# Performance work log

Hardware: AMD Instinct MI355X
Metric: run time of the kernel (lower is better)

The kernel has to match this reference:

```python
import jax, jax.numpy as jnp
import numpy as np

LAYERS, BLOCKS = 10, 4
RES_CH, END_CH, CLASSES, GROUPS = 32, 256, 256, 1
BN_EPS = 1e-5


def conv1x1(x, w, b):
    # x: (bn, Cin, L), w: (Cout, Cin), b: (Cout,)
    return jnp.einsum('oc,bcl->bol', w, x) + b[None, :, None]


def mish(x):
    return x * jnp.tanh(jax.nn.softplus(x))


def concat_mish(x):
    return mish(jnp.concatenate((x, -x), axis=1))


def channel_shuffle(x, groups):
    if groups == 1:
        return x
    bn, c, l = x.shape
    return x.reshape(bn, groups, c // groups, l).transpose(0, 2, 1, 3).reshape(bn, c, l)


def batchnorm_train(x, g, b):
    # BatchNorm1d in training mode: per-channel stats over (batch, length), biased var
    m = jnp.mean(x, axis=(0, 2), keepdims=True)
    v = jnp.mean((x - m) ** 2, axis=(0, 2), keepdims=True)
    return (x - m) * jax.lax.rsqrt(v + BN_EPS) * g[None, :, None] + b[None, :, None]


def dilate(x, dilation, init_dilation, pad_start=True):
    bn, c, l = x.shape
    if dilation == 1:
        x = jnp.transpose(x, (1, 2, 0)).reshape(c, l * init_dilation, bn // init_dilation)
        return jnp.transpose(x, (2, 0, 1))
    f = dilation // init_dilation
    if f == 1:
        return x
    new_l = (l + f - 1) // f * f
    if new_l != l:
        pad = (new_l - l, 0) if pad_start else (0, new_l - l)
        x = jnp.pad(x, ((0, 0), (0, 0), pad))
        l = new_l
    l //= f
    bn *= f
    x = jnp.transpose(x, (1, 2, 0)).reshape(c, l, bn)
    return jnp.transpose(x, (2, 0, 1))


def setup_inputs() -> dict:
    key = jax.random.key(0)
    ks = iter(jax.random.split(key, 32))
    nl = LAYERS * BLOCKS
    f32 = jnp.float32
    inp = {
        'x': jax.random.normal(next(ks), (8, CLASSES, 8192), dtype=f32),
        'start_w': jax.random.normal(next(ks), (RES_CH, CLASSES), dtype=f32) * 0.05,
        'start_b': jnp.zeros((RES_CH,), f32),
        'gate_w': jax.random.normal(next(ks), (nl, RES_CH // 2, RES_CH), dtype=f32) * 0.15,
        'gate_b': jnp.zeros((nl, RES_CH // 2), f32),
        'res_w': jax.random.normal(next(ks), (nl, RES_CH, RES_CH), dtype=f32) * 0.15,
        'res_b': jnp.zeros((nl, RES_CH), f32),
        'bn_g': jnp.ones((nl, RES_CH), f32),
        'bn_b': jnp.zeros((nl, RES_CH), f32),
        'end_bn1_g': jnp.ones((RES_CH,), f32),
        'end_bn1_b': jnp.zeros((RES_CH,), f32),
        'end_conv1_w': jax.random.normal(next(ks), (END_CH // 2, 2 * RES_CH), dtype=f32) * 0.1,
        'end_conv1_b': jnp.zeros((END_CH // 2,), f32),
        'end_bn2_g': jnp.ones((END_CH // 2,), f32),
        'end_bn2_b': jnp.zeros((END_CH // 2,), f32),
        'end_conv2_w': jax.random.normal(next(ks), (CLASSES, END_CH), dtype=f32) * 0.05,
        'end_conv2_b': jnp.zeros((CLASSES,), f32),
    }
    return inp


def reference(x, start_w, start_b, gate_w, gate_b, res_w, res_b, bn_g, bn_b,
              end_bn1_g, end_bn1_b, end_conv1_w, end_conv1_b,
              end_bn2_g, end_bn2_b, end_conv2_w, end_conv2_b):
    x = conv1x1(x, start_w, start_b)
    prev_dilation = 1
    i = 0
    for block in range(BLOCKS):
        for layer in range(LAYERS):
            x = dilate(x, 2 ** layer, prev_dilation)
            prev_dilation = 2 ** layer
            x0 = x
            h = concat_mish(conv1x1(x, gate_w[i], gate_b[i]))
            h = channel_shuffle(h, GROUPS)
            h = batchnorm_train(conv1x1(h, res_w[i], res_b[i]), bn_g[i], bn_b[i])
            h = channel_shuffle(h, GROUPS)
            x = x0 + h
            i += 1
    x = concat_mish(batchnorm_train(x, end_bn1_g, end_bn1_b))
    x = concat_mish(batchnorm_train(conv1x1(x, end_conv1_w, end_conv1_b), end_bn2_g, end_bn2_b))
    x = conv1x1(x, end_conv2_w, end_conv2_b)
    x = dilate(x, 1, 2 ** (LAYERS - 1))
    return x
```

## Files before the change

kernel.cpp:

```cpp
#include <hip/hip_runtime.h>

#define BS 256
#define NBLK 256
#define STATS_F   0
#define W2T_F     46080
#define XBUF_F    131072
#define RBUF_F    2228224
#define WS_NEED_BYTES (4325376ull * 4ull)
#define CNTS_U  4096

__device__ __forceinline__ void mish2(float v, float& mp, float& mn) {
  float vc = fminf(fmaxf(v, -30.f), 30.f);
  float u  = __expf(vc);
  float n1 = u * (u + 2.f);
  mp = v * n1 * __builtin_amdgcn_rcpf(n1 + 2.f);
  float n2 = fmaf(2.f, u, 1.f);
  float d2 = fmaf(2.f * u, u, n2);
  mn = -v * n2 * __builtin_amdgcn_rcpf(d2);
}

__device__ __forceinline__ float coherent_ld(const float* p) {
  return __hip_atomic_load(p, __ATOMIC_RELAXED, __HIP_MEMORY_SCOPE_AGENT);
}
__device__ __forceinline__ void coherent_st(float* p, float v) {
  __hip_atomic_store(p, v, __ATOMIC_RELAXED, __HIP_MEMORY_SCOPE_AGENT);
}

__device__ __forceinline__ void block_reduce_stats(const float (&vals)[32],
    float* s_red, float* s_p2, float* slot, int t) {
  #pragma unroll
  for (int cc = 0; cc < 8; ++cc) {
    float4 v = make_float4(vals[cc*4+0], vals[cc*4+1], vals[cc*4+2], vals[cc*4+3]);
    *(float4*)(&s_red[t*32 + ((cc ^ (t & 7)) << 2)]) = v;
  }
  __syncthreads();
  {
    int q = t & 63, grp = t >> 6, c = q & 31;
    bool issq = (q >= 32);
    float acc = 0.f;
    #pragma clang loop unroll_count(8)
    for (int rr = 0; rr < 64; ++rr) {
      int row = grp * 64 + rr;
      float v = s_red[row*32 + ((((c >> 2) ^ (row & 7)) << 2) | (c & 3))];
      acc = fmaf(v, issq ? v : 1.f, acc);
    }
    s_p2[t] = acc;
  }
  __syncthreads();
  if (t < 64) {
    float tot = s_p2[t] + s_p2[t+64] + s_p2[t+128] + s_p2[t+192];
    unsafeAtomicAdd(&slot[(blockIdx.x & 15) * 64 + t], tot);
  }
  __syncthreads();
}

__device__ __forceinline__ void bn32_from_slot(const float* slot, const float* g,
    const float* b, float* sA, float* sB, float* s_tmp, int t) {
  if (t < 64) {
    float s = 0.f;
    #pragma unroll
    for (int rep = 0; rep < 16; ++rep) s += slot[rep*64 + t];
    s_tmp[t] = s;
  }
  __syncthreads();
  if (t < 32) {
    float mean = s_tmp[t] * (1.f/65536.f);
    float var  = fmaf(-mean, mean, s_tmp[t+32] * (1.f/65536.f));
    float sc   = g[t] * rsqrtf(var + 1e-5f);
    sA[t] = sc;
    sB[t] = fmaf(-mean, sc, b[t]);
  }
  __syncthreads();
}

__device__ __forceinline__ void bn32_slot_coh(const float* slot, const float* g,
    const float* b, float* sA, float* sB, float* s_tmp, int t) {
  if (t < 64) {
    float s = 0.f;
    #pragma unroll
    for (int rep = 0; rep < 16; ++rep) s += coherent_ld(&slot[rep*64 + t]);
    s_tmp[t] = s;
  }
  __syncthreads();
  if (t < 32) {
    float mean = s_tmp[t] * (1.f/65536.f);
    float var  = fmaf(-mean, mean, s_tmp[t+32] * (1.f/65536.f));
    float sc   = g[t] * rsqrtf(var + 1e-5f);
    sA[t] = sc;
    sB[t] = fmaf(-mean, sc, b[t]);
  }
  __syncthreads();
}

__device__ __forceinline__ void layer_convs(const float (&x)[32], float (&r)[32],
    const float* gw, const float* gb, const float* rw, const float* rb, int i) {
  float g[16];
  #pragma unroll
  for (int j = 0; j < 16; ++j) g[j] = gb[i*16 + j];
  #pragma unroll
  for (int j = 0; j < 16; ++j)
    #pragma unroll
    for (int k = 0; k < 32; ++k)
      g[j] = fmaf(gw[i*512 + j*32 + k], x[k], g[j]);
  float cm[32];
  #pragma unroll
  for (int j = 0; j < 16; ++j) mish2(g[j], cm[j], cm[j+16]);
  #pragma unroll
  for (int j = 0; j < 32; ++j) r[j] = rb[i*32 + j];
  #pragma unroll
  for (int j = 0; j < 32; ++j)
    #pragma unroll
    for (int k = 0; k < 32; ++k)
      r[j] = fmaf(rw[i*1024 + j*32 + k], cm[k], r[j]);
}

__device__ __forceinline__ void grid_sync_p(float* base, unsigned gen, bool flush) {
  __syncthreads();
  unsigned* flags = (unsigned*)base;
  unsigned* cnts  = (unsigned*)base + CNTS_U;
  if (blockIdx.x == 0) {
    if (threadIdx.x == 0) {
      if (flush) __threadfence();
      __hip_atomic_fetch_add(&cnts[0], 1u, __ATOMIC_RELAXED, __HIP_MEMORY_SCOPE_AGENT);
      unsigned sum;
      do {
        __builtin_amdgcn_s_sleep(2);
        sum = 0;
        #pragma unroll
        for (int x = 0; x < 32; ++x)
          sum += __hip_atomic_load(&cnts[x*16], __ATOMIC_RELAXED, __HIP_MEMORY_SCOPE_AGENT);
      } while (sum < gen * NBLK);
    }
    __syncthreads();
    __hip_atomic_store(&flags[threadIdx.x * 16], gen,
                       __ATOMIC_RELAXED, __HIP_MEMORY_SCOPE_AGENT);
  } else {
    if (threadIdx.x == 0) {
      if (flush) __threadfence();
      __hip_atomic_fetch_add(&cnts[(blockIdx.x & 31) * 16], 1u,
                             __ATOMIC_RELAXED, __HIP_MEMORY_SCOPE_AGENT);
      while (__hip_atomic_load(&flags[blockIdx.x * 16],
                               __ATOMIC_RELAXED, __HIP_MEMORY_SCOPE_AGENT) < gen)
        __builtin_amdgcn_s_sleep(2);
    }
    __syncthreads();
  }
}

extern "C" __global__ void __launch_bounds__(BS, 1)
qnet_p(const float* __restrict__ xin, const float* __restrict__ sw,
       const float* __restrict__ sb, const float* __restrict__ gw,
       const float* __restrict__ gb, const float* __restrict__ rw,
       const float* __restrict__ rb, const float* __restrict__ bng,
       const float* __restrict__ bnb, const float* __restrict__ e1g,
       const float* __restrict__ e1b, const float* __restrict__ c1w,
       const float* __restrict__ c1b, const float* __restrict__ c2w,
       float* __restrict__ ws)
{
  __shared__ float s_red[BS*32];
  __shared__ float s_p2[BS];
  __shared__ float s_A[32], s_B[32], s_tmp[64];
  const int t = threadIdx.x, p = blockIdx.x * BS + t;
  float* stats = ws + STATS_F;
  float* w2t   = ws + W2T_F;
  float* xb    = ws + XBUF_F;
  float* syncb = ws + RBUF_F;
  unsigned gen = 0;
  { int o = p & 255, kk = p >> 8; w2t[kk*256 + o] = c2w[o*256 + kk]; }
  const int bb = p >> 13, ll = p & 8191;
  const int pbase = bb * 2097152 + ll;
  float x[32];
  #pragma unroll
  for (int j = 0; j < 32; ++j) x[j] = sb[j];
  #pragma clang loop unroll(disable)
  for (int c8 = 0; c8 < 32; ++c8) {
    float xv[8];
    #pragma unroll
    for (int cc = 0; cc < 8; ++cc) xv[cc] = xin[pbase + (c8*8+cc)*8192];
    #pragma unroll
    for (int j = 0; j < 32; ++j)
      #pragma unroll
      for (int cc = 0; cc < 8; ++cc)
        x[j] = fmaf(sw[j*256 + c8*8 + cc], xv[cc], x[j]);
  }
  float r[32];
  layer_convs(x, r, gw, gb, rw, rb, 0);
  block_reduce_stats(r, s_red, s_p2, stats + 0, t);
  ++gen; grid_sync_p(syncb, gen, false);
  #pragma clang loop unroll(disable)
  for (int i = 1; i < 40; ++i) {
    bn32_slot_coh(stats + (i-1)*1024, bng + (i-1)*32, bnb + (i-1)*32, s_A, s_B, s_tmp, t);
    #pragma unroll
    for (int c = 0; c < 32; ++c) x[c] += fmaf(r[c], s_A[c], s_B[c]);
    layer_convs(x, r, gw, gb, rw, rb, i);
    block_reduce_stats(r, s_red, s_p2, stats + i*1024, t);
    ++gen; grid_sync_p(syncb, gen, false);
  }
  bn32_slot_coh(stats + 39*1024, bng + 39*32, bnb + 39*32, s_A, s_B, s_tmp, t);
  #pragma unroll
  for (int c = 0; c < 32; ++c) {
    x[c] += fmaf(r[c], s_A[c], s_B[c]);
    xb[c*65536 + p] = x[c];
  }
  block_reduce_stats(x, s_red, s_p2, stats + 40*1024, t);
  ++gen; grid_sync_p(syncb, gen, false);
  bn32_slot_coh(stats + 40*1024, e1g, e1b, s_A, s_B, s_tmp, t);
  float mp[32], mn[32];
  #pragma unroll
  for (int c = 0; c < 32; ++c) {
    float xh = fmaf(x[c], s_A[c], s_B[c]);
    mish2(xh, mp[c], mn[c]);
  }
  #pragma clang loop unroll(disable)
  for (int pp = 0; pp < 4; ++pp) {
    float zc[32];
    #pragma unroll
    for (int j = 0; j < 32; ++j) zc[j] = c1b[pp*32 + j];
    #pragma unroll
    for (int j = 0; j < 32; ++j)
      #pragma unroll
      for (int k = 0; k < 32; ++k) {
        zc[j] = fmaf(c1w[(pp*32+j)*64 + k],      mp[k], zc[j]);
        zc[j] = fmaf(c1w[(pp*32+j)*64 + 32 + k], mn[k], zc[j]);
      }
    block_reduce_stats(zc, s_red, s_p2, stats + (41+pp)*1024, t);
  }
}

__global__ void __launch_bounds__(BS, 2) k_end3(const float* __restrict__ e1g,
    const float* __restrict__ e1b, const float* __restrict__ c1w,
    const float* __restrict__ c1b, const float* __restrict__ e2g,
    const float* __restrict__ e2b, const float* __restrict__ c2b,
    float* __restrict__ out, float* __restrict__ ws) {
  __shared__ float s_A[32], s_B[32], s_tmp[64];
  __shared__ float s_A2[128], s_B2[128];
  __shared__ float s_ck[2048];
  __shared__ float4 wbuf4[512];
  __shared__ float s_c1b[128];
  __shared__ float s_c2b[32];
  int t = threadIdx.x;
  const int pA = blockIdx.x * 512 + t;
  const int pB = pA + 256;
  float* stats = ws + STATS_F; float* xb = ws + XBUF_F;
  const float* w2t = ws + W2T_F;
  const int ocb = blockIdx.y * 32;
  if (t < 32) ((float4*)s_c1b)[t] = ((const float4*)c1b)[t];
  else if (t < 40) ((float4*)s_c2b)[t-32] = ((const float4*)(c2b + ocb))[t-32];
  bn32_from_slot(stats + 40*1024, e1g, e1b, s_A, s_B, s_tmp, t);
  if (t < 128) {
    int pp = t >> 5, c = t & 31;
    const float* sl = stats + (41+pp)*1024;
    float S = 0.f, Q = 0.f;
    #pragma unroll
    for (int rep = 0; rep < 16; ++rep) { S += sl[rep*64 + c]; Q += sl[rep*64 + 32 + c]; }
    float mean = S * (1.f/65536.f);
    float var  = fmaf(-mean, mean, Q * (1.f/65536.f));
    float sc   = e2g[t] * rsqrtf(var + 1e-5f);
    s_A2[t] = sc;
    s_B2[t] = fmaf(-mean, sc, e2b[t]);
  }
  __syncthreads();
  float mpA[32], mnA[32], mpB[32], mnB[32];
  #pragma unroll
  for (int c = 0; c < 32; ++c) {
    float xhA = fmaf(xb[c*65536 + pA], s_A[c], s_B[c]);
    mish2(xhA, mpA[c], mnA[c]);
    float xhB = fmaf(xb[c*65536 + pB], s_A[c], s_B[c]);
    mish2(xhB, mpB[c], mnB[c]);
  }
  float acc[64];
  #pragma unroll
  for (int o = 0; o < 32; ++o) { acc[o] = s_c2b[o]; acc[32+o] = s_c2b[o]; }
  #pragma clang loop unroll(disable)
  for (int kc = 0; kc < 4; ++kc) {
    __syncthreads();
    { const float4* cs = (const float4*)(c1w + kc*2048);
      ((float4*)s_ck)[t]       = cs[t];
      ((float4*)s_ck)[256 + t] = cs[256 + t]; }
    #pragma unroll
    for (int q = 0; q < 2; ++q) {
      int f = q*256 + t;
      int r = f >> 3, o4 = f & 7;
      int kglob = (r < 32) ? (kc*32 + r) : (96 + kc*32 + r);
      wbuf4[f] = *((const float4*)(w2t + kglob*256 + ocb) + o4);
    }
    __syncthreads();
    #pragma clang loop unroll_count(2)
    for (int j = 0; j < 32; ++j) {
      const int k = kc*32 + j;
      float zA = s_c1b[k], zB = s_c1b[k];
      const float4* cw = (const float4*)&s_ck[j*64];
      #pragma unroll
      for (int k4 = 0; k4 < 8; ++k4) {
        float4 a = cw[k4], b = cw[8+k4];
        zA = fmaf(a.x, mpA[k4*4+0], zA);
        zA = fmaf(a.y, mpA[k4*4+1], zA);
        zA = fmaf(a.z, mpA[k4*4+2], zA);
        zA = fmaf(a.w, mpA[k4*4+3], zA);
        zA = fmaf(b.x, mnA[k4*4+0], zA);
        zA = fmaf(b.y, mnA[k4*4+1], zA);
        zA = fmaf(b.z, mnA[k4*4+2], zA);
        zA = fmaf(b.w, mnA[k4*4+3], zA);
        zB = fmaf(a.x, mpB[k4*4+0], zB);
        zB = fmaf(a.y, mpB[k4*4+1], zB);
        zB = fmaf(a.z, mpB[k4*4+2], zB);
        zB = fmaf(a.w, mpB[k4*4+3], zB);
        zB = fmaf(b.x, mnB[k4*4+0], zB);
        zB = fmaf(b.y, mnB[k4*4+1], zB);
        zB = fmaf(b.z, mnB[k4*4+2], zB);
        zB = fmaf(b.w, mnB[k4*4+3], zB);
      }
      float zhA = fmaf(zA, s_A2[k], s_B2[k]);
      float mpvA, mnvA; mish2(zhA, mpvA, mnvA);
      float zhB = fmaf(zB, s_A2[k], s_B2[k]);
      float mpvB, mnvB; mish2(zhB, mpvB, mnvB);
      const float4* w0 = &wbuf4[j*8];
      const float4* w1 = &wbuf4[(32 + j)*8];
      #pragma unroll
      for (int o4 = 0; o4 < 8; ++o4) {
        float4 a = w0[o4], b = w1[o4];
        acc[o4*4+0] = fmaf(a.x, mpvA, fmaf(b.x, mnvA, acc[o4*4+0]));
        acc[o4*4+1] = fmaf(a.y, mpvA, fmaf(b.y, mnvA, acc[o4*4+1]));
        acc[o4*4+2] = fmaf(a.z, mpvA, fmaf(b.z, mnvA, acc[o4*4+2]));
        acc[o4*4+3] = fmaf(a.w, mpvA, fmaf(b.w, mnvA, acc[o4*4+3]));
        acc[32+o4*4+0] = fmaf(a.x, mpvB, fmaf(b.x, mnvB, acc[32+o4*4+0]));
        acc[32+o4*4+1] = fmaf(a.y, mpvB, fmaf(b.y, mnvB, acc[32+o4*4+1]));
        acc[32+o4*4+2] = fmaf(a.z, mpvB, fmaf(b.z, mnvB, acc[32+o4*4+2]));
        acc[32+o4*4+3] = fmaf(a.w, mpvB, fmaf(b.w, mnvB, acc[32+o4*4+3]));
      }
    }
  }
  {
    int bbA = pA >> 13, llA = pA & 8191;
    int obA = bbA * 2097152 + ocb * 8192 + llA;
    #pragma unroll
    for (int o = 0; o < 32; ++o) out[obA + o*8192] = acc[o];
    int bbB = pB >> 13, llB = pB & 8191;
    int obB = bbB * 2097152 + ocb * 8192 + llB;
    #pragma unroll
    for (int o = 0; o < 32; ++o) out[obB + o*8192] = acc[32+o];
  }
}

#define W2T_FB  4608
#define STATS_OUT_OFF (8u*1024u*1024u)
#define SLOT_STRIDE 16384

__device__ __forceinline__ void grid_sync_fb(float* ws, unsigned gen, bool flush) {
  grid_sync_p(ws, gen, flush);
}
__device__ __forceinline__ void brs_fb(const float (&vals)[32],
    float* s_red, float* s_p2, float* slot, int t) {
  #pragma unroll
  for (int cc = 0; cc < 8; ++cc) {
    float4 v = make_float4(vals[cc*4+0], vals[cc*4+1], vals[cc*4+2], vals[cc*4+3]);
    *(float4*)(&s_red[t*32 + ((cc ^ (t & 7)) << 2)]) = v;
  }
  __syncthreads();
  {
    int q = t & 63, grp = t >> 6, c = q & 31;
    bool issq = (q >= 32);
    float acc = 0.f;
    #pragma clang loop unroll_count(8)
    for (int rr = 0; rr < 64; ++rr) {
      int row = grp * 64 + rr;
      float v = s_red[row*32 + ((((c >> 2) ^ (row & 7)) << 2) | (c & 3))];
      acc = fmaf(v, issq ? v : 1.f, acc);
    }
    s_p2[t] = acc;
  }
  __syncthreads();
  if (t < 64) {
    float tot = s_p2[t] + s_p2[t+64] + s_p2[t+128] + s_p2[t+192];
    coherent_st(&slot[blockIdx.x * 64 + t], tot);
  }
}

extern "C" __global__ void __launch_bounds__(BS, 1)
qnet_fb(const float* __restrict__ xin,
        const float* __restrict__ sw, const float* __restrict__ sb,
        const float* __restrict__ gw, const float* __restrict__ gb,
        const float* __restrict__ rw, const float* __restrict__ rb,
        const float* __restrict__ bng, const float* __restrict__ bnb,
        const float* __restrict__ e1g, const float* __restrict__ e1b,
        const float* __restrict__ c1w, const float* __restrict__ c1b,
        const float* __restrict__ e2g, const float* __restrict__ e2b,
        const float* __restrict__ c2w, const float* __restrict__ c2b,
        float* __restrict__ out, float* __restrict__ ws)
{
  __shared__ float s_red[BS*32];
  __shared__ float s_p2[BS];
  __shared__ float s_tot[64];
  __shared__ float s_bcA[128];
  __shared__ float s_bcB[128];
  const int t = threadIdx.x;
  const int p = blockIdx.x * BS + t;
  float* w2t = ws + W2T_FB;
  float* zg  = out;
  float* sg  = out + STATS_OUT_OFF;
  unsigned gen = 0;
  const int bb = p >> 13, ll = p & 8191;
  const int pbase = bb * 2097152 + ll;
  { int o = p & 255, kk = p >> 8; coherent_st(&w2t[kk*256 + o], c2w[o*256 + kk]); }
  float x[32];
  #pragma unroll
  for (int j = 0; j < 32; ++j) x[j] = sb[j];
  #pragma clang loop unroll(disable)
  for (int c8 = 0; c8 < 32; ++c8) {
    float xv[8];
    #pragma unroll
    for (int cc = 0; cc < 8; ++cc) xv[cc] = xin[pbase + (c8*8+cc)*8192];
    #pragma unroll
    for (int j = 0; j < 32; ++j)
      #pragma unroll
      for (int cc = 0; cc < 8; ++cc)
        x[j] = fmaf(sw[j*256 + c8*8 + cc], xv[cc], x[j]);
  }
  #pragma clang loop unroll(disable)
  for (int i = 0; i < 40; ++i) {
    float r[32];
    layer_convs(x, r, gw, gb, rw, rb, i);
    brs_fb(r, s_red, s_p2, sg + (size_t)i * SLOT_STRIDE, t);
    ++gen; grid_sync_fb(ws, gen, false);
    {
      int q = t & 63, w = t >> 6;
      const float* col = sg + (size_t)i * SLOT_STRIDE + q;
      float acc2 = 0.f;
      #pragma clang loop unroll_count(16)
      for (int j = 0; j < 64; ++j) acc2 += coherent_ld(&col[(w*64+j)*64]);
      s_p2[t] = acc2;
    }
    __syncthreads();
    if (t < 64) s_tot[t] = s_p2[t] + s_p2[t+64] + s_p2[t+128] + s_p2[t+192];
    __syncthreads();
    if (t < 32) {
      float mean = s_tot[t] * (1.f/65536.f);
      float var  = fmaf(-mean, mean, s_tot[t+32] * (1.f/65536.f));
      float sc   = bng[i*32+t] * rsqrtf(var + 1e-5f);
      s_bcA[t] = sc;
      s_bcB[t] = fmaf(-mean, sc, bnb[i*32+t]);
    }
    __syncthreads();
    #pragma unroll
    for (int c = 0; c < 32; ++c) x[c] += fmaf(r[c], s_bcA[c], s_bcB[c]);
  }
  brs_fb(x, s_red, s_p2, sg + 40 * SLOT_STRIDE, t);
  ++gen; grid_sync_fb(ws, gen, false);
  {
    int q = t & 63, w = t >> 6;
    const float* col = sg + (size_t)40 * SLOT_STRIDE + q;
    float acc2 = 0.f;
    #pragma clang loop unroll_count(16)
    for (int j = 0; j < 64; ++j) acc2 += coherent_ld(&col[(w*64+j)*64]);
    s_p2[t] = acc2;
  }
  __syncthreads();
  if (t < 64) s_tot[t] = s_p2[t] + s_p2[t+64] + s_p2[t+128] + s_p2[t+192];
  __syncthreads();
  if (t < 32) {
    float mean = s_tot[t] * (1.f/65536.f);
    float var  = fmaf(-mean, mean, s_tot[t+32] * (1.f/65536.f));
    float sc   = e1g[t] * rsqrtf(var + 1e-5f);
    s_bcA[t] = sc;
    s_bcB[t] = fmaf(-mean, sc, e1b[t]);
  }
  __syncthreads();
  float mp[32], mn[32];
  #pragma unroll
  for (int c = 0; c < 32; ++c) {
    float xh = fmaf(x[c], s_bcA[c], s_bcB[c]);
    mish2(xh, mp[c], mn[c]);
  }
  #pragma clang loop unroll(disable)
  for (int pp = 0; pp < 4; ++pp) {
    float zc[32];
    #pragma unroll
    for (int j = 0; j < 32; ++j) zc[j] = c1b[pp*32 + j];
    #pragma unroll
    for (int j = 0; j < 32; ++j)
      #pragma unroll
      for (int k = 0; k < 32; ++k) {
        zc[j] = fmaf(c1w[(pp*32+j)*64 + k],      mp[k], zc[j]);
        zc[j] = fmaf(c1w[(pp*32+j)*64 + 32 + k], mn[k], zc[j]);
      }
    #pragma unroll
    for (int j = 0; j < 32; ++j) zg[(pp*32+j)*65536 + p] = zc[j];
    brs_fb(zc, s_red, s_p2, sg + (size_t)(41+pp) * SLOT_STRIDE, t);
    __syncthreads();
  }
  ++gen; grid_sync_fb(ws, gen, false);
  {
    int slot = 41 + (t >> 6), q = t & 63;
    const float* col = sg + (size_t)slot * SLOT_STRIDE + q;
    float acc2 = 0.f;
    #pragma clang loop unroll_count(32)
    for (int b2 = 0; b2 < 256; ++b2) acc2 += coherent_ld(&col[b2*64]);
    s_p2[t] = acc2;
  }
  __syncthreads();
  if (t < 128) {
    float S = s_p2[((t>>5)<<6) | (t&31)];
    float Q = s_p2[((t>>5)<<6) | 32 | (t&31)];
    float mean = S * (1.f/65536.f);
    float var  = fmaf(-mean, mean, Q * (1.f/65536.f));
    float sc   = e2g[t] * rsqrtf(var + 1e-5f);
    s_bcA[t] = sc;
    s_bcB[t] = fmaf(-mean, sc, e2b[t]);
  }
  __syncthreads();
  float acc[256];
  #pragma unroll
  for (int o = 0; o < 256; ++o) acc[o] = c2b[o];
  float zv_next = zg[p];
  #pragma clang loop unroll(disable)
  for (int k = 0; k < 128; ++k) {
    float zv = zv_next;
    zv_next = zg[((k+1)&127)*65536 + p];
    float zh = fmaf(zv, s_bcA[k], s_bcB[k]);
    float mpv, mnv; mish2(zh, mpv, mnv);
    const float* w0 = &w2t[k*256];
    const float* w1 = &w2t[(k+128)*256];
    #pragma unroll
    for (int o = 0; o < 256; ++o)
      acc[o] = fmaf(w0[o], mpv, fmaf(w1[o], mnv, acc[o]));
  }
  ++gen; grid_sync_fb(ws, gen, true);
  #pragma unroll
  for (int o = 0; o < 256; ++o)
    out[bb*2097152 + o*8192 + ll] = acc[o];
}

extern "C" void kernel_launch(void* const* d_in, const int* in_sizes, int n_in,
                              void* d_out, int out_size, void* d_ws, size_t ws_size,
                              hipStream_t stream) {
  const float* xin = (const float*)d_in[0];
  const float* sw  = (const float*)d_in[1];
  const float* sb  = (const float*)d_in[2];
  const float* gw  = (const float*)d_in[3];
  const float* gb  = (const float*)d_in[4];
  const float* rw  = (const float*)d_in[5];
  const float* rb  = (const float*)d_in[6];
  const float* bng = (const float*)d_in[7];
  const float* bnb = (const float*)d_in[8];
  const float* e1g = (const float*)d_in[9];
  const float* e1b = (const float*)d_in[10];
  const float* c1w = (const float*)d_in[11];
  const float* c1b = (const float*)d_in[12];
  const float* e2g = (const float*)d_in[13];
  const float* e2b = (const float*)d_in[14];
  const float* c2w = (const float*)d_in[15];
  const float* c2b = (const float*)d_in[16];
  float* out = (float*)d_out;
  float* ws  = (float*)d_ws;

  if (ws_size >= WS_NEED_BYTES) {
    hipMemsetAsync(d_ws, 0, 45 * 1024 * 4, stream);
    hipMemsetAsync((char*)d_ws + (size_t)RBUF_F * 4, 0, 4608 * 4, stream);
    void* args[] = { &xin, &sw, &sb, &gw, &gb, &rw, &rb, &bng, &bnb,
                     &e1g, &e1b, &c1w, &c1b, &c2w, &ws };
    hipError_t err = hipLaunchCooperativeKernel((const void*)qnet_p,
                                                dim3(NBLK), dim3(BS), args, 0, stream);
    if (err != hipSuccess) {
      hipLaunchKernelGGL(qnet_p, dim3(NBLK), dim3(BS), 0, stream,
                         xin, sw, sb, gw, gb, rw, rb, bng, bnb,
                         e1g, e1b, c1w, c1b, c2w, ws);
    }
    k_end3<<<dim3(128, 8), BS, 0, stream>>>(e1g, e1b, c1w, c1b, e2g, e2b, c2b, out, ws);
  } else {
    hipMemsetAsync(d_ws, 0, (CNTS_U + 512) * 4, stream);
    void* args[] = { &xin, &sw, &sb, &gw, &gb, &rw, &rb, &bng, &bnb,
                     &e1g, &e1b, &c1w, &c1b, &e2g, &e2b, &c2w, &c2b, &out, &ws };
    hipError_t err = hipLaunchCooperativeKernel((const void*)qnet_fb,
                                                dim3(NBLK), dim3(BS), args, 0, stream);
    if (err != hipSuccess) {
      hipLaunchKernelGGL(qnet_fb, dim3(NBLK), dim3(BS), 0, stream,
                         xin, sw, sb, gw, gb, rw, rb, bng, bnb,
                         e1g, e1b, c1w, c1b, e2g, e2b, c2w, c2b, out, ws);
    }
  }
}
```

Measured before the change: 1.434 ms.

## Use 128 blocks of 512 threads with a flagless all-poll grid barrier

The persistent cooperative kernel is relaunched as 128 blocks of 512 threads instead of 256 blocks of 256. The block-level stats reduction is templated on thread count to match. The grid barrier is replaced by a lean version where every block adds to a striped counter and polls the summed counters itself, with no leader block or flag broadcast. This halves the number of barrier participants and removes one propagation hop per layer. In exchange it puts more waves and LDS on fewer CUs, which may leave half the CUs idle, and every block now polls 32 counters at once.

New measurement: 1.510 ms. 1.05x slower.

```diff
diff --git a/kernel.cpp b/kernel.cpp
--- a/kernel.cpp
+++ b/kernel.cpp
@@ -1,6 +1,8 @@
 #include <hip/hip_runtime.h>
 
 #define BS 256
+#define BSP 512
+#define NBLKP 128
 #define NBLK 256
 #define STATS_F   0
 #define W2T_F     46080
@@ -26,6 +28,7 @@
   __hip_atomic_store(p, v, __ATOMIC_RELAXED, __HIP_MEMORY_SCOPE_AGENT);
 }
 
+template<int NT>
 __device__ __forceinline__ void block_reduce_stats(const float (&vals)[32],
     float* s_red, float* s_p2, float* slot, int t) {
   #pragma unroll
@@ -48,7 +51,9 @@
   }
   __syncthreads();
   if (t < 64) {
-    float tot = s_p2[t] + s_p2[t+64] + s_p2[t+128] + s_p2[t+192];
+    float tot = 0.f;
+    #pragma unroll
+    for (int g = 0; g < NT/64; ++g) tot += s_p2[t + g*64];
     unsafeAtomicAdd(&slot[(blockIdx.x & 15) * 64 + t], tot);
   }
   __syncthreads();
@@ -112,6 +117,24 @@
     #pragma unroll
     for (int k = 0; k < 32; ++k)
       r[j] = fmaf(rw[i*1024 + j*32 + k], cm[k], r[j]);
+}
+
+__device__ __forceinline__ void grid_sync_lean(float* base, unsigned gen) {
+  __syncthreads();
+  unsigned* cnts = (unsigned*)base + CNTS_U;
+  if (threadIdx.x == 0) {
+    __hip_atomic_fetch_add(&cnts[(blockIdx.x & 31) * 16], 1u,
+                           __ATOMIC_RELAXED, __HIP_MEMORY_SCOPE_AGENT);
+    unsigned sum;
+    do {
+      __builtin_amdgcn_s_sleep(1);
+      sum = 0;
+      #pragma unroll
+      for (int x = 0; x < 32; ++x)
+        sum += __hip_atomic_load(&cnts[x*16], __ATOMIC_RELAXED, __HIP_MEMORY_SCOPE_AGENT);
+    } while (sum < gen * NBLKP);
+  }
+  __syncthreads();
 }
 
 __device__ __forceinline__ void grid_sync_p(float* base, unsigned gen, bool flush) {
@@ -147,7 +170,7 @@
   }
 }
 
-extern "C" __global__ void __launch_bounds__(BS, 1)
+extern "C" __global__ void __launch_bounds__(BSP, 1)
 qnet_p(const float* __restrict__ xin, const float* __restrict__ sw,
        const float* __restrict__ sb, const float* __restrict__ gw,
        const float* __restrict__ gb, const float* __restrict__ rw,
@@ -157,10 +180,10 @@
        const float* __restrict__ c1b, const float* __restrict__ c2w,
        float* __restrict__ ws)
 {
-  __shared__ float s_red[BS*32];
-  __shared__ float s_p2[BS];
+  __shared__ float s_red[BSP*32];
+  __shared__ float s_p2[BSP];
   __shared__ float s_A[32], s_B[32], s_tmp[64];
-  const int t = threadIdx.x, p = blockIdx.x * BS + t;
+  const int t = threadIdx.x, p = blockIdx.x * BSP + t;
   float* stats = ws + STATS_F;
   float* w2t   = ws + W2T_F;
   float* xb    = ws + XBUF_F;
@@ -185,16 +208,16 @@
   }
   float r[32];
   layer_convs(x, r, gw, gb, rw, rb, 0);
-  block_reduce_stats(r, s_red, s_p2, stats + 0, t);
-  ++gen; grid_sync_p(syncb, gen, false);
+  block_reduce_stats<BSP>(r, s_red, s_p2, stats + 0, t);
+  ++gen; grid_sync_lean(syncb, gen);
   #pragma clang loop unroll(disable)
   for (int i = 1; i < 40; ++i) {
     bn32_slot_coh(stats + (i-1)*1024, bng + (i-1)*32, bnb + (i-1)*32, s_A, s_B, s_tmp, t);
     #pragma unroll
     for (int c = 0; c < 32; ++c) x[c] += fmaf(r[c], s_A[c], s_B[c]);
     layer_convs(x, r, gw, gb, rw, rb, i);
-    block_reduce_stats(r, s_red, s_p2, stats + i*1024, t);
-    ++gen; grid_sync_p(syncb, gen, false);
+    block_reduce_stats<BSP>(r, s_red, s_p2, stats + i*1024, t);
+    ++gen; grid_sync_lean(syncb, gen);
   }
   bn32_slot_coh(stats + 39*1024, bng + 39*32, bnb + 39*32, s_A, s_B, s_tmp, t);
   #pragma unroll
@@ -202,8 +225,8 @@
     x[c] += fmaf(r[c], s_A[c], s_B[c]);
     xb[c*65536 + p] = x[c];
   }
-  block_reduce_stats(x, s_red, s_p2, stats + 40*1024, t);
-  ++gen; grid_sync_p(syncb, gen, false);
+  block_reduce_stats<BSP>(x, s_red, s_p2, stats + 40*1024, t);
+  ++gen; grid_sync_lean(syncb, gen);
   bn32_slot_coh(stats + 40*1024, e1g, e1b, s_A, s_B, s_tmp, t);
   float mp[32], mn[32];
   #pragma unroll
@@ -223,7 +246,7 @@
         zc[j] = fmaf(c1w[(pp*32+j)*64 + k],      mp[k], zc[j]);
         zc[j] = fmaf(c1w[(pp*32+j)*64 + 32 + k], mn[k], zc[j]);
       }
-    block_reduce_stats(zc, s_red, s_p2, stats + (41+pp)*1024, t);
+    block_reduce_stats<BSP>(zc, s_red, s_p2, stats + (41+pp)*1024, t);
   }
 }
 
@@ -559,9 +582,9 @@
     void* args[] = { &xin, &sw, &sb, &gw, &gb, &rw, &rb, &bng, &bnb,
                      &e1g, &e1b, &c1w, &c1b, &c2w, &ws };
     hipError_t err = hipLaunchCooperativeKernel((const void*)qnet_p,
-                                                dim3(NBLK), dim3(BS), args, 0, stream);
+                                                dim3(NBLKP), dim3(BSP), args, 0, stream);
     if (err != hipSuccess) {
-      hipLaunchKernelGGL(qnet_p, dim3(NBLK), dim3(BS), 0, stream,
+      hipLaunchKernelGGL(qnet_p, dim3(NBLKP), dim3(BSP), 0, stream,
                          xin, sw, sb, gw, gb, rw, rb, bng, bnb,
                          e1g, e1b, c1w, c1b, c2w, ws);
     }
```
